# Performance work log

Hardware: AMD Instinct MI355X
Metric: run time of the kernel (lower is better)

Reference implementation:

```python
import jax, jax.numpy as jnp
import numpy as np

N_ENT = 16384   # num_entities
N_REL = 50      # num relations
D = 128         # embedding dim
B = 4           # num bases
E = 262144      # num edges (avg degree 16)


def setup_inputs() -> dict:
    key = jax.random.key(0)
    k1, k2, k3, k4, k5, k6 = jax.random.split(key, 6)
    x = jax.random.normal(k1, (N_ENT, D), dtype=jnp.float32)
    bases = jax.random.normal(k2, (B, D, D), dtype=jnp.float32) * 0.05
    comps = jax.random.normal(k3, (N_REL, B), dtype=jnp.float32)
    alpha = jax.random.normal(k4, (N_REL, 1), dtype=jnp.float32)
    edge_index = jax.random.randint(k5, (2, E), 0, N_ENT, dtype=jnp.int64)
    edge_type = jax.random.randint(k6, (E,), 0, N_REL, dtype=jnp.int64)
    return {"x": x, "bases": bases, "comps": comps, "alpha": alpha,
            "edge_index": edge_index, "edge_type": edge_type}


def reference(x, bases, comps, alpha, edge_index, edge_type):
    # R-GCN basis-decomposition message passing:
    #   msg_e = (h_j @ W_{r(e)}) * alpha_{r(e)} * norm_e,  W_r = sum_b comps[r,b] * bases[b]
    #   out_i = sum_{e: row(e)=i} msg_e
    n = x.shape[0]
    row, col = edge_index[0], edge_index[1]

    # edge_norm = 1/sqrt(D_row) * 1/sqrt(D_col) with out-degree over rows
    ones = jnp.ones(row.shape, x.dtype)
    deg = jax.ops.segment_sum(ones, row, num_segments=n)
    deg_inv = jnp.where(deg > 0, jax.lax.rsqrt(jnp.maximum(deg, 1.0)), 0.0)
    norm = deg_inv[row] * deg_inv[col]               # [E]

    h_j = x[col]                                     # [E, D] gather
    c_e = comps[edge_type]                           # [E, B] gather
    # sum_b c[e,b] * (h_j[e] @ bases[b])  ==  einsum over (b,d)
    hj_b = c_e[:, :, None] * h_j[:, None, :]         # [E, B, D]
    msg = jnp.einsum('ebd,bdf->ef', hj_b, bases)     # [E, D] big GEMM
    msg = msg * alpha[edge_type] * norm[:, None]

    out = jax.ops.segment_sum(msg, row, num_segments=n)  # scatter-add to nodes
    return out
```

## Files before the change

### kernel.cpp

```cpp
#include <hip/hip_runtime.h>
#include <stdint.h>

#define NENT 16384
#define NREL 50
#define NE   262144
#define BSTR 64
#define ASTR 260

typedef __attribute__((ext_vector_type(8))) short short8;
typedef __attribute__((ext_vector_type(4))) float float4v;

__device__ __forceinline__ float bf2f(uint32_t u){ return __uint_as_float(u << 16); }
__device__ __forceinline__ uint32_t fpack(float a, float b){
  uint32_t ua = __float_as_uint(a), ub = __float_as_uint(b);
  ua = (ua + 0x7fffu + ((ua >> 16) & 1u)) >> 16;
  ub = (ub + 0x7fffu + ((ub >> 16) & 1u)) >> 16;
  return ua | (ub << 16);
}
__device__ __forceinline__ unsigned short f2bf(float a){
  uint32_t ua = __float_as_uint(a);
  return (unsigned short)((ua + 0x7fffu + ((ua >> 16) & 1u)) >> 16);
}
__device__ __forceinline__ float rdlane_f(float v, int j){
  return __uint_as_float((uint32_t)__builtin_amdgcn_readlane((int)__float_as_uint(v), j));
}

__global__ void k_prep0(int* __restrict__ deg,
                        const float* __restrict__ alpha, const float* __restrict__ comps,
                        float* __restrict__ acomb,
                        const float* __restrict__ W, unsigned short* __restrict__ WT,
                        const float* __restrict__ x, uint32_t* __restrict__ xbf){
  int gid = blockIdx.x * 256 + threadIdx.x;
  if (gid < NENT) deg[gid] = 0;
  if (gid < NREL * 4) acomb[gid] = alpha[gid >> 2] * comps[gid];
  {
    int n = gid >> 9, k = gid & 511;
    WT[gid] = f2bf(W[k * 128 + n]);
  }
  {
    const float4* xin = (const float4*)(x + gid * 32);
    uint32_t* xo = xbf + gid * 16;
    #pragma unroll
    for (int j = 0; j < 8; ++j){
      float4 p = xin[j];
      xo[j * 2]     = fpack(p.x, p.y);
      xo[j * 2 + 1] = fpack(p.z, p.w);
    }
  }
}

__global__ void k_fill_bkt(const int* __restrict__ eidx, const int* __restrict__ etype,
                           int* __restrict__ deg, uint32_t* __restrict__ bucket){
  int e = blockIdx.x * 256 + threadIdx.x;
  int row = eidx[e], col = eidx[NE + e], r = etype[e];
  int pos = atomicAdd(&deg[row], 1);
  if (pos < BSTR) bucket[row * BSTR + pos] = (uint32_t)col | ((uint32_t)r << 14);
}

__global__ __launch_bounds__(256) void k_fused(
    const uint32_t* __restrict__ xbf, const int* __restrict__ deg,
    const float* __restrict__ acomb, const uint32_t* __restrict__ bucket,
    const unsigned short* __restrict__ WT, float* __restrict__ outf)
{
  __shared__ uint32_t A_lds[16 * ASTR];
  int t = threadIdx.x, lane = t & 63, wv = t >> 6;
  int row0 = blockIdx.x * 16;

  for (int rr = wv * 4; rr < wv * 4 + 4; ++rr){
    int i = row0 + rr;
    int d = deg[i];
    uint32_t* Arow = &A_lds[rr * ASTR];
    if (d == 0){
      Arow[lane] = 0; Arow[lane+64] = 0; Arow[lane+128] = 0; Arow[lane+192] = 0;
      continue;
    }
    int de = min(d, BSTR);
    float di = rsqrtf((float)d);
    uint32_t rec = bucket[i * BSTR + min(lane, de - 1)];
    int colL = (int)(rec & 0x3FFFu);
    int rL   = (int)(rec >> 14);
    int dc   = deg[colL];
    float wL = (lane < de && dc > 0) ? di * rsqrtf((float)dc) : 0.f;
    float4 ac = ((const float4*)acomb)[rL];
    float w0 = wL*ac.x, w1 = wL*ac.y, w2 = wL*ac.z, w3 = wL*ac.w;
    float a0=0,a1=0,a2=0,a3=0,a4=0,a5=0,a6=0,a7=0;
    int rde = (de + 3) & ~3;
    for (int j = 0; j < rde; j += 4){
      #pragma unroll
      for (int jj = 0; jj < 4; ++jj){
        int   cj = __builtin_amdgcn_readlane(colL, j + jj);
        float m0 = rdlane_f(w0, j + jj), m1 = rdlane_f(w1, j + jj);
        float m2 = rdlane_f(w2, j + jj), m3 = rdlane_f(w3, j + jj);
        uint32_t hv = xbf[cj * 64 + lane];
        float h0 = bf2f(hv & 0xffffu), h1 = bf2f(hv >> 16);
        a0 += m0*h0; a1 += m0*h1;
        a2 += m1*h0; a3 += m1*h1;
        a4 += m2*h0; a5 += m2*h1;
        a6 += m3*h0; a7 += m3*h1;
      }
    }
    Arow[lane]       = fpack(a0, a1);
    Arow[lane + 64]  = fpack(a2, a3);
    Arow[lane + 128] = fpack(a4, a5);
    Arow[lane + 192] = fpack(a6, a7);
  }
  __syncthreads();

  int m16 = lane & 15, quad = lane >> 4;
  int c0 = (wv * 2) * 16 + m16, c1 = c0 + 16;
  const short8* B0 = (const short8*)(WT + c0 * 512);
  const short8* B1 = (const short8*)(WT + c1 * 512);
  const uint32_t* Abase = &A_lds[m16 * ASTR];
  float4v acc0 = {0.f,0.f,0.f,0.f}, acc1 = {0.f,0.f,0.f,0.f};
  #pragma unroll
  for (int k0 = 0; k0 < 512; k0 += 32){
    short8 aF = *(const short8*)&Abase[(k0 >> 1) + quad * 4];
    int idx = (k0 >> 3) + quad;
    acc0 = __builtin_amdgcn_mfma_f32_16x16x32_bf16(aF, B0[idx], acc0, 0, 0, 0);
    acc1 = __builtin_amdgcn_mfma_f32_16x16x32_bf16(aF, B1[idx], acc1, 0, 0, 0);
  }
  int mrow = row0 + quad * 4;
  #pragma unroll
  for (int r = 0; r < 4; ++r){
    outf[(mrow + r) * 128 + c0] = acc0[r];
    outf[(mrow + r) * 128 + c1] = acc1[r];
  }
}

extern "C" void kernel_launch(void* const* d_in, const int* in_sizes, int n_in,
                              void* d_out, int out_size, void* d_ws, size_t ws_size,
                              hipStream_t stream){
  (void)in_sizes; (void)n_in; (void)out_size; (void)ws_size;
  const float* x     = (const float*)d_in[0];
  const float* bases = (const float*)d_in[1];
  const float* comps = (const float*)d_in[2];
  const float* alpha = (const float*)d_in[3];
  const int* eidx    = (const int*)d_in[4];
  const int* etype   = (const int*)d_in[5];
  char* ws = (char*)d_ws;

  int*      deg    = (int*)      (ws + 0);
  float*    acomb  = (float*)    (ws + (64  << 10));
  unsigned short* WT = (unsigned short*)(ws + (128 << 10));
  uint32_t* xbf    = (uint32_t*) (ws + (512 << 10));
  uint32_t* bucket = (uint32_t*) (ws + (5u  << 20));

  k_prep0   <<<256, 256, 0, stream>>>(deg, alpha, comps, acomb, bases, WT, x, xbf);
  k_fill_bkt<<<NE / 256, 256, 0, stream>>>(eidx, etype, deg, bucket);
  k_fused   <<<NENT / 16, 256, 0, stream>>>(xbf, deg, acomb, bucket, WT, (float*)d_out);
}
```

Measured before the change: 119.7 us.

## Merge three kernels into one cooperative kernel with grid-wide syncs

Replaces the prep, bucket-fill and fused gather/GEMM kernels with a single cooperative kernel of 1024 blocks that uses grid syncs between phases. The aim is to remove two kernel launch gaps and boundaries. The prep work is redistributed across more threads, each converting 8 floats of x instead of 32. In exchange it relies on all 1024 blocks of 256 threads being co-resident (launch bounds of 4 blocks per CU on 256 CUs), and grid syncs carry their own overhead.

```diff
diff --git a/kernel.cpp b/kernel.cpp
--- a/kernel.cpp
+++ b/kernel.cpp
@@ -1,5 +1,8 @@
 #include <hip/hip_runtime.h>
+#include <hip/hip_cooperative_groups.h>
 #include <stdint.h>
+
+namespace cg = cooperative_groups;
 
 #define NENT 16384
 #define NREL 50
@@ -25,47 +28,41 @@
   return __uint_as_float((uint32_t)__builtin_amdgcn_readlane((int)__float_as_uint(v), j));
 }
 
-__global__ void k_prep0(int* __restrict__ deg,
-                        const float* __restrict__ alpha, const float* __restrict__ comps,
-                        float* __restrict__ acomb,
-                        const float* __restrict__ W, unsigned short* __restrict__ WT,
-                        const float* __restrict__ x, uint32_t* __restrict__ xbf){
-  int gid = blockIdx.x * 256 + threadIdx.x;
+__global__ __launch_bounds__(256, 4) void k_all(
+    const float* __restrict__ x, const float* __restrict__ W,
+    const float* __restrict__ comps, const float* __restrict__ alpha,
+    const int* __restrict__ eidx, const int* __restrict__ etype,
+    int* __restrict__ deg, float* __restrict__ acomb,
+    unsigned short* __restrict__ WT, uint32_t* __restrict__ xbf,
+    uint32_t* __restrict__ bucket, float* __restrict__ outf)
+{
+  __shared__ uint32_t A_lds[16 * ASTR];
+  int t = threadIdx.x, lane = t & 63, wv = t >> 6;
+  int gid = blockIdx.x * 256 + t;
+
   if (gid < NENT) deg[gid] = 0;
   if (gid < NREL * 4) acomb[gid] = alpha[gid >> 2] * comps[gid];
-  {
+  if (gid < 65536){
     int n = gid >> 9, k = gid & 511;
     WT[gid] = f2bf(W[k * 128 + n]);
   }
   {
-    const float4* xin = (const float4*)(x + gid * 32);
-    uint32_t* xo = xbf + gid * 16;
-    #pragma unroll
-    for (int j = 0; j < 8; ++j){
-      float4 p = xin[j];
-      xo[j * 2]     = fpack(p.x, p.y);
-      xo[j * 2 + 1] = fpack(p.z, p.w);
-    }
+    const float4* xin4 = (const float4*)x;
+    float4 p0 = xin4[gid * 2], p1 = xin4[gid * 2 + 1];
+    uint32_t* xo = xbf + gid * 4;
+    xo[0] = fpack(p0.x, p0.y); xo[1] = fpack(p0.z, p0.w);
+    xo[2] = fpack(p1.x, p1.y); xo[3] = fpack(p1.z, p1.w);
   }
-}
+  cg::this_grid().sync();
 
-__global__ void k_fill_bkt(const int* __restrict__ eidx, const int* __restrict__ etype,
-                           int* __restrict__ deg, uint32_t* __restrict__ bucket){
-  int e = blockIdx.x * 256 + threadIdx.x;
-  int row = eidx[e], col = eidx[NE + e], r = etype[e];
-  int pos = atomicAdd(&deg[row], 1);
-  if (pos < BSTR) bucket[row * BSTR + pos] = (uint32_t)col | ((uint32_t)r << 14);
-}
+  {
+    int row = eidx[gid], col = eidx[NE + gid], r = etype[gid];
+    int pos = atomicAdd(&deg[row], 1);
+    if (pos < BSTR) bucket[row * BSTR + pos] = (uint32_t)col | ((uint32_t)r << 14);
+  }
+  cg::this_grid().sync();
 
-__global__ __launch_bounds__(256) void k_fused(
-    const uint32_t* __restrict__ xbf, const int* __restrict__ deg,
-    const float* __restrict__ acomb, const uint32_t* __restrict__ bucket,
-    const unsigned short* __restrict__ WT, float* __restrict__ outf)
-{
-  __shared__ uint32_t A_lds[16 * ASTR];
-  int t = threadIdx.x, lane = t & 63, wv = t >> 6;
   int row0 = blockIdx.x * 16;
-
   for (int rr = wv * 4; rr < wv * 4 + 4; ++rr){
     int i = row0 + rr;
     int d = deg[i];
@@ -144,8 +141,12 @@
   unsigned short* WT = (unsigned short*)(ws + (128 << 10));
   uint32_t* xbf    = (uint32_t*) (ws + (512 << 10));
   uint32_t* bucket = (uint32_t*) (ws + (5u  << 20));
+  float*    outf   = (float*)d_out;
 
-  k_prep0   <<<256, 256, 0, stream>>>(deg, alpha, comps, acomb, bases, WT, x, xbf);
-  k_fill_bkt<<<NE / 256, 256, 0, stream>>>(eidx, etype, deg, bucket);
-  k_fused   <<<NENT / 16, 256, 0, stream>>>(xbf, deg, acomb, bucket, WT, (float*)d_out);
+  void* args[] = { (void*)&x, (void*)&bases, (void*)&comps, (void*)&alpha,
+                   (void*)&eidx, (void*)&etype,
+                   (void*)&deg, (void*)&acomb, (void*)&WT, (void*)&xbf,
+                   (void*)&bucket, (void*)&outf };
+  hipLaunchCooperativeKernel((const void*)k_all, dim3(NENT / 16), dim3(256),
+                             args, 0, stream);
 }
```

Result: slower. 318.0 us (+165.6%).
